# Kernel optimization log

Hardware: AMD Instinct MI355X
Metric: run time of the kernel (lower is better)

The kernel has to match this reference:

```python
import jax, jax.numpy as jnp
import numpy as np

N_COLORS = 8192

def setup_inputs() -> dict:
    key = jax.random.key(0)
    k1, k2, k3 = jax.random.split(key, 3)
    action = jax.random.uniform(k1, (N_COLORS,), dtype=jnp.float32)
    holding = jax.random.uniform(k2, (N_COLORS,), dtype=jnp.float32)
    dominos = jax.random.uniform(k3, (N_COLORS, N_COLORS), dtype=jnp.float32)
    return {"action": action, "holding": holding, "dominos": dominos}


def reference(action, holding, dominos):
    # Probabilistic (noisy-OR over proofs) semantics of the Scallop program,
    # the dense differentiable limit of difftopkproofs provenance.
    #
    # next_holding(n) = OR_m [ current_holding(m) AND current_domino(m,n) ] AND action(n)
    # proofs[m, n] = holding[m] * dominos[m, n]
    proofs = holding[:, None] * dominos                      # [m, n]
    next_holding = action * (1.0 - jnp.prod(1.0 - proofs, axis=0))  # [n]

    # next_domino(n,m): two proofs, combined by noisy-OR
    #   p1 = dominos[n,m] * (1 - action[m])
    #   p2 = dominos[n,m] * (1 - holding[n])
    p1 = dominos * (1.0 - action)[None, :]                   # [n, m]
    p2 = dominos * (1.0 - holding)[:, None]                  # [n, m]
    next_domino = 1.0 - (1.0 - p1) * (1.0 - p2)              # [n, m]

    return next_holding, next_domino
```

## Files before the change

### kernel.cpp

```cpp
#include <hip/hip_runtime.h>


typedef float v4f __attribute__((ext_vector_type(4)));

template<int ROWS, int THREADS, int CHUNKS>
__global__ __launch_bounds__(THREADS, 4) void wm_linear(
    const float* __restrict__ action,
    const float* __restrict__ holding,
    const float* __restrict__ dominos,
    float* __restrict__ out_d,
    float* __restrict__ ws,
    int n)
{
    __shared__ float sh_h[ROWS];
    __shared__ float sh_hr[ROWS];

    const int tid = threadIdx.x;
    const int b   = blockIdx.x;
    const int r0  = b * ROWS;
    if (tid < ROWS) {
        const float h = holding[r0 + tid];
        sh_h[tid]  = h;
        sh_hr[tid] = 1.0f - h;
    }
    __syncthreads();

    const v4f ones = {1.0f, 1.0f, 1.0f, 1.0f};

    v4f av[CHUNKS], ac[CHUNKS], prod[CHUNKS];
    #pragma unroll
    for (int k = 0; k < CHUNKS; ++k) {
        const int c = k * THREADS * 4 + tid * 4;
        av[k]   = *reinterpret_cast<const v4f*>(action + c);
        ac[k]   = ones - av[k];
        prod[k] = ones;
    }

    const float* src = dominos + (size_t)r0 * (size_t)n;
    float*       dst = out_d   + (size_t)r0 * (size_t)n;

    #pragma unroll 2
    for (int r = 0; r < ROWS; ++r) {
        const float h  = sh_h[r];
        const float hr = sh_hr[r];

        v4f v[CHUNKS];
        #pragma unroll
        for (int k = 0; k < CHUNKS; ++k) {
            v[k] = __builtin_nontemporal_load(reinterpret_cast<const v4f*>(
                src + (size_t)r * (size_t)n + k * THREADS * 4 + tid * 4));
        }
        #pragma unroll
        for (int k = 0; k < CHUNKS; ++k) {
            prod[k] *= (ones - v[k] * h);
            const v4f p1 = v[k] * ac[k];
            const v4f p2 = v[k] * hr;
            const v4f o  = p1 + p2 - p1 * p2;
            __builtin_nontemporal_store(o, reinterpret_cast<v4f*>(
                dst + (size_t)r * (size_t)n + k * THREADS * 4 + tid * 4));
        }
    }

    #pragma unroll
    for (int k = 0; k < CHUNKS; ++k) {
        *reinterpret_cast<v4f*>(ws + (size_t)b * (size_t)n + k * THREADS * 4 + tid * 4) = prod[k];
    }
}

__global__ __launch_bounds__(256) void wm_reduce_col(
    const float* __restrict__ action,
    const float* __restrict__ ws,
    float* __restrict__ out_h,
    int n, int K)
{
    const int c = blockIdx.x * blockDim.x + threadIdx.x;
    if (c >= n) return;

    float prod = 1.0f;
    #pragma unroll 4
    for (int k = 0; k < K; ++k) {
        prod *= ws[(size_t)k * (size_t)n + c];
    }
    out_h[c] = action[c] * (1.0f - prod);
}


__global__ __launch_bounds__(256) void wm_main_generic(
    const float* __restrict__ action,
    const float* __restrict__ holding,
    const float* __restrict__ dominos,
    float* __restrict__ out_d,
    float* __restrict__ ws,
    float* __restrict__ out_h,
    int n, int rows_per_chunk)
{
    const int c4 = (blockIdx.x * blockDim.x + threadIdx.x) * 4;
    if (c4 >= n) return;

    const int r0 = blockIdx.y * rows_per_chunk;
    int r1 = r0 + rows_per_chunk;
    if (r1 > n) r1 = n;

    const float4 av = *reinterpret_cast<const float4*>(action + c4);
    const float4 ac = make_float4(1.0f - av.x, 1.0f - av.y, 1.0f - av.z, 1.0f - av.w);

    v4f prod = {1.0f, 1.0f, 1.0f, 1.0f};

    #pragma unroll 8
    for (int r = r0; r < r1; ++r) {
        const float h  = holding[r];
        const float hr = 1.0f - h;
        const size_t off = (size_t)r * (size_t)n + (size_t)c4;
        const v4f v = __builtin_nontemporal_load(
            reinterpret_cast<const v4f*>(dominos + off));

        prod.x *= fmaf(-h, v.x, 1.0f);
        prod.y *= fmaf(-h, v.y, 1.0f);
        prod.z *= fmaf(-h, v.z, 1.0f);
        prod.w *= fmaf(-h, v.w, 1.0f);

        v4f o;
        { float p1 = v.x * ac.x, p2 = v.x * hr; o.x = fmaf(-p1, p2, p1 + p2); }
        { float p1 = v.y * ac.y, p2 = v.y * hr; o.y = fmaf(-p1, p2, p1 + p2); }
        { float p1 = v.z * ac.z, p2 = v.z * hr; o.z = fmaf(-p1, p2, p1 + p2); }
        { float p1 = v.w * ac.w, p2 = v.w * hr; o.w = fmaf(-p1, p2, p1 + p2); }
        __builtin_nontemporal_store(o, reinterpret_cast<v4f*>(out_d + off));
    }

    if (ws) {
        *reinterpret_cast<v4f*>(ws + (size_t)blockIdx.y * (size_t)n + (size_t)c4) = prod;
    } else {
        float4 oh;
        oh.x = av.x * (1.0f - prod.x);
        oh.y = av.y * (1.0f - prod.y);
        oh.z = av.z * (1.0f - prod.z);
        oh.w = av.w * (1.0f - prod.w);
        *reinterpret_cast<float4*>(out_h + c4) = oh;
    }
}

extern "C" void kernel_launch(void* const* d_in, const int* in_sizes, int n_in,
                              void* d_out, int out_size, void* d_ws, size_t ws_size,
                              hipStream_t stream)
{
    const int n = in_sizes[0];
    const float* action  = (const float*)d_in[0];
    const float* holding = (const float*)d_in[1];
    const float* dominos = (const float*)d_in[2];

    float* out_h = (float*)d_out;
    float* out_d = out_h + n;
    float* ws    = (float*)d_ws;

    constexpr int ROWS    = 32;
    constexpr int THREADS = 1024;

    const bool fast =
        (n % (THREADS * 4) == 0) &&
        (n % ROWS == 0) &&
        ((size_t)(n / ROWS) * (size_t)n * sizeof(float) <= ws_size) &&
        (n / (THREADS * 4) == 2);

    if (fast) {
        const int nblocks = n / ROWS;
        wm_linear<ROWS, THREADS, 2><<<nblocks, THREADS, 0, stream>>>(
            action, holding, dominos, out_d, ws, n);
        wm_reduce_col<<<(n + 255) / 256, 256, 0, stream>>>(
            action, ws, out_h, n, nblocks);
    } else {
        const int cols_per_block = 256 * 4;
        const int cb = (n + cols_per_block - 1) / cols_per_block;

        const size_t max_rb_ws = ws_size / ((size_t)n * sizeof(float));
        int rb = 256;
        while (rb > 1 && ((size_t)rb > max_rb_ws || rb > n)) rb >>= 1;
        if (max_rb_ws < 1) rb = 1;

        const int rows_per_chunk = (n + rb - 1) / rb;
        const bool use_ws = (rb > 1);

        dim3 grid1(cb, rb);
        wm_main_generic<<<grid1, 256, 0, stream>>>(action, holding, dominos,
                                                   out_d,
                                                   use_ws ? ws : nullptr,
                                                   out_h,
                                                   n, rows_per_chunk);
        if (use_ws) {
            wm_reduce_col<<<(n + 255) / 256, 256, 0, stream>>>(
                action, ws, out_h, n, rb);
        }
    }
}
```

Measured before the change: 117.5 us.

## Split main kernel blocks across column halves and parallelize column reduction over K

The main streaming kernel now gives each 1024-thread block one column half of a 32-row group instead of both halves. This doubles the block count to 512 and raises the launch-bounds occupancy hint from 4 to 8 blocks per CU, while each thread carries fewer live registers. The column-product reduction over the 256 partial rows is split across 8 thread groups per column, combined in shared memory, so more threads work on the short serial reduction. The trade-off is more blocks and a shared-memory barrier in exchange for better parallelism and latency hiding on a bandwidth-bound stream.

Result: faster. 110.3 us (-6.2%).

```diff
diff --git a/kernel.cpp b/kernel.cpp
--- a/kernel.cpp
+++ b/kernel.cpp
@@ -3,8 +3,8 @@
 
 typedef float v4f __attribute__((ext_vector_type(4)));
 
-template<int ROWS, int THREADS, int CHUNKS>
-__global__ __launch_bounds__(THREADS, 4) void wm_linear(
+template<int ROWS, int THREADS, int COLSPLIT>
+__global__ __launch_bounds__(THREADS, 8) void wm_split(
     const float* __restrict__ action,
     const float* __restrict__ holding,
     const float* __restrict__ dominos,
@@ -17,7 +17,11 @@
 
     const int tid = threadIdx.x;
     const int b   = blockIdx.x;
-    const int r0  = b * ROWS;
+    const int rg  = b / COLSPLIT;
+    const int ch  = b % COLSPLIT;
+    const int r0  = rg * ROWS;
+    const int c0  = ch * (n / COLSPLIT);
+
     if (tid < ROWS) {
         const float h = holding[r0 + tid];
         sh_h[tid]  = h;
@@ -26,62 +30,63 @@
     __syncthreads();
 
     const v4f ones = {1.0f, 1.0f, 1.0f, 1.0f};
-
-    v4f av[CHUNKS], ac[CHUNKS], prod[CHUNKS];
-    #pragma unroll
-    for (int k = 0; k < CHUNKS; ++k) {
-        const int c = k * THREADS * 4 + tid * 4;
-        av[k]   = *reinterpret_cast<const v4f*>(action + c);
-        ac[k]   = ones - av[k];
-        prod[k] = ones;
-    }
-
-    const float* src = dominos + (size_t)r0 * (size_t)n;
-    float*       dst = out_d   + (size_t)r0 * (size_t)n;
-
-    #pragma unroll 2
+    const int  c   = c0 + tid * 4;
+
+    const v4f av   = *reinterpret_cast<const v4f*>(action + c);
+    const v4f ac   = ones - av;
+    v4f prod       = ones;
+
+    const float* src = dominos + (size_t)r0 * (size_t)n + c;
+    float*       dst = out_d   + (size_t)r0 * (size_t)n + c;
+
+    #pragma unroll 4
     for (int r = 0; r < ROWS; ++r) {
         const float h  = sh_h[r];
         const float hr = sh_hr[r];
 
-        v4f v[CHUNKS];
-        #pragma unroll
-        for (int k = 0; k < CHUNKS; ++k) {
-            v[k] = __builtin_nontemporal_load(reinterpret_cast<const v4f*>(
-                src + (size_t)r * (size_t)n + k * THREADS * 4 + tid * 4));
-        }
-        #pragma unroll
-        for (int k = 0; k < CHUNKS; ++k) {
-            prod[k] *= (ones - v[k] * h);
-            const v4f p1 = v[k] * ac[k];
-            const v4f p2 = v[k] * hr;
-            const v4f o  = p1 + p2 - p1 * p2;
-            __builtin_nontemporal_store(o, reinterpret_cast<v4f*>(
-                dst + (size_t)r * (size_t)n + k * THREADS * 4 + tid * 4));
-        }
-    }
-
-    #pragma unroll
-    for (int k = 0; k < CHUNKS; ++k) {
-        *reinterpret_cast<v4f*>(ws + (size_t)b * (size_t)n + k * THREADS * 4 + tid * 4) = prod[k];
-    }
-}
-
-__global__ __launch_bounds__(256) void wm_reduce_col(
+        const v4f v = __builtin_nontemporal_load(
+            reinterpret_cast<const v4f*>(src + (size_t)r * (size_t)n));
+
+        prod *= (ones - v * h);
+        const v4f p1 = v * ac;
+        const v4f p2 = v * hr;
+        const v4f o  = p1 + p2 - p1 * p2;
+        __builtin_nontemporal_store(o,
+            reinterpret_cast<v4f*>(dst + (size_t)r * (size_t)n));
+    }
+
+    *reinterpret_cast<v4f*>(ws + (size_t)rg * (size_t)n + c) = prod;
+}
+
+template<int KSPLIT, int COLS>
+__global__ __launch_bounds__(KSPLIT * COLS) void wm_reduce_par(
     const float* __restrict__ action,
     const float* __restrict__ ws,
     float* __restrict__ out_h,
     int n, int K)
 {
-    const int c = blockIdx.x * blockDim.x + threadIdx.x;
-    if (c >= n) return;
-
+    __shared__ float sh[KSPLIT][COLS];
+
+    const int tid = threadIdx.x;
+    const int cl  = tid % COLS;
+    const int kk  = tid / COLS;
+    const int c   = blockIdx.x * COLS + cl;
+
+    const int kchunk = K / KSPLIT;
     float prod = 1.0f;
     #pragma unroll 4
-    for (int k = 0; k < K; ++k) {
+    for (int k = kk * kchunk; k < (kk + 1) * kchunk; ++k) {
         prod *= ws[(size_t)k * (size_t)n + c];
     }
-    out_h[c] = action[c] * (1.0f - prod);
+    sh[kk][cl] = prod;
+    __syncthreads();
+
+    if (kk == 0) {
+        float p = sh[0][cl];
+        #pragma unroll
+        for (int j = 1; j < KSPLIT; ++j) p *= sh[j][cl];
+        out_h[c] = action[c] * (1.0f - p);
+    }
 }
 
 
@@ -139,6 +144,23 @@
     }
 }
 
+__global__ __launch_bounds__(256) void wm_reduce_col(
+    const float* __restrict__ action,
+    const float* __restrict__ ws,
+    float* __restrict__ out_h,
+    int n, int K)
+{
+    const int c = blockIdx.x * blockDim.x + threadIdx.x;
+    if (c >= n) return;
+
+    float prod = 1.0f;
+    #pragma unroll 4
+    for (int k = 0; k < K; ++k) {
+        prod *= ws[(size_t)k * (size_t)n + c];
+    }
+    out_h[c] = action[c] * (1.0f - prod);
+}
+
 extern "C" void kernel_launch(void* const* d_in, const int* in_sizes, int n_in,
                               void* d_out, int out_size, void* d_ws, size_t ws_size,
                               hipStream_t stream)
@@ -152,21 +174,27 @@
     float* out_d = out_h + n;
     float* ws    = (float*)d_ws;
 
-    constexpr int ROWS    = 32;
-    constexpr int THREADS = 1024;
+    constexpr int ROWS     = 32;
+    constexpr int THREADS  = 1024;
+    constexpr int COLSPLIT = 2;
+    constexpr int KSPLIT   = 8;
+    constexpr int COLS     = 32;
+
+    const int K = n / ROWS;
 
     const bool fast =
-        (n % (THREADS * 4) == 0) &&
         (n % ROWS == 0) &&
-        ((size_t)(n / ROWS) * (size_t)n * sizeof(float) <= ws_size) &&
-        (n / (THREADS * 4) == 2);
+        (n / COLSPLIT == THREADS * 4) &&
+        (K % KSPLIT == 0) &&
+        (n % COLS == 0) &&
+        ((size_t)K * (size_t)n * sizeof(float) <= ws_size);
 
     if (fast) {
-        const int nblocks = n / ROWS;
-        wm_linear<ROWS, THREADS, 2><<<nblocks, THREADS, 0, stream>>>(
+        const int nblocks = K * COLSPLIT;
+        wm_split<ROWS, THREADS, COLSPLIT><<<nblocks, THREADS, 0, stream>>>(
             action, holding, dominos, out_d, ws, n);
-        wm_reduce_col<<<(n + 255) / 256, 256, 0, stream>>>(
-            action, ws, out_h, n, nblocks);
+        wm_reduce_par<KSPLIT, COLS><<<n / COLS, KSPLIT * COLS, 0, stream>>>(
+            action, ws, out_h, n, K);
     } else {
         const int cols_per_block = 256 * 4;
         const int cb = (n + cols_per_block - 1) / cols_per_block;
```
